# Optimization experiments

Measured on AMD Instinct MI355X. Metric: run time of the kernel, lower is better.

Reference implementation:

```python
import jax, jax.numpy as jnp
import numpy as np

T = 2048      # total tokens (single prefill sequence)
HID = 2048    # hidden_size
H = 16        # num k-heads == num v-heads
DK = 128      # key head dim
DV = 128      # value head dim
K = 4         # causal conv kernel width
EPS = 1e-6


def setup_inputs() -> dict:
    key = jax.random.key(0)
    ks = jax.random.split(key, 10)
    n = lambda k, shape, sc: (jax.random.normal(k, shape, jnp.float32) * sc)
    return {
        "hidden_states": n(ks[0], (T, HID), 1.0),
        "Wq": n(ks[1], (HID, H * DK), 0.02),
        "Wk": n(ks[2], (HID, H * DK), 0.02),
        "Wv": n(ks[3], (HID, H * DV), 0.02),
        "Wb": n(ks[4], (HID, H), 0.02),
        "conv_wq": n(ks[5], (H * DK, K), 0.5),
        "conv_wk": n(ks[6], (H * DK, K), 0.5),
        "conv_wv": n(ks[7], (H * DV, K), 0.5),
        "o_norm_w": jnp.ones((DV,), jnp.float32),
        "Wo": n(ks[8], (HID, HID), 0.02),
    }


def _causal_conv_silu(x, w):
    # x: [T, D], w: [D, K] depthwise causal conv, then SiLU (matches causal_conv1d_fn)
    xp = jnp.pad(x, ((K - 1, 0), (0, 0)))
    y = sum(xp[j:j + T] * w[:, j] for j in range(K))
    return jax.nn.silu(y)


def _l2norm(x):
    return x * jax.lax.rsqrt(jnp.sum(x * x, axis=-1, keepdims=True) + EPS)


def reference(hidden_states, Wq, Wk, Wv, Wb, conv_wq, conv_wk, conv_wv, o_norm_w, Wo):
    # projections [T, H*D]
    q = _causal_conv_silu(hidden_states @ Wq, conv_wq).reshape(T, H, DK)
    k = _causal_conv_silu(hidden_states @ Wk, conv_wk).reshape(T, H, DK)
    v = _causal_conv_silu(hidden_states @ Wv, conv_wv).reshape(T, H, DV)
    beta = jax.nn.sigmoid(hidden_states @ Wb)  # [T, H]

    # qk l2-norm + scale (FLA chunk_delta_rule defaults)
    q = _l2norm(q) * (DK ** -0.5)
    k = _l2norm(k)

    # delta-rule recurrence: S <- S + beta * k (v - k^T S)
    def step(S, inp):
        q_t, k_t, v_t, b_t = inp            # [H,DK],[H,DK],[H,DV],[H]
        kS = jnp.einsum('hk,hkv->hv', k_t, S)
        delta = b_t[:, None] * (v_t - kS)   # [H, DV]
        S = S + jnp.einsum('hk,hv->hkv', k_t, delta)
        o_t = jnp.einsum('hk,hkv->hv', q_t, S)
        return S, o_t

    S0 = jnp.zeros((H, DK, DV), jnp.float32)
    _, o = jax.lax.scan(step, S0, (q, k, v, beta))  # o: [T, H, DV]

    # per-head RMSNorm on value head dim
    o = o * jax.lax.rsqrt(jnp.mean(o * o, axis=-1, keepdims=True) + EPS) * o_norm_w
    out = o.reshape(T, H * DV) @ Wo
    return out
```

## Files before the change

kernel.cpp:

```cpp
#include <hip/hip_runtime.h>

typedef unsigned short u16;
typedef __attribute__((ext_vector_type(4))) unsigned short u16x4;
typedef __attribute__((ext_vector_type(8))) unsigned short u16x8;
typedef __attribute__((ext_vector_type(8))) short short8;
typedef __attribute__((ext_vector_type(4))) float f32x4;

#define DEVI __device__ __forceinline__

DEVI u16 f2b(float f) {
  union { float f; unsigned u; } x; x.f = f;
  unsigned r = (x.u + 0x7fffu + ((x.u >> 16) & 1u)) >> 16;
  return (u16)r;
}
DEVI float b2f(u16 h) {
  union { unsigned u; float f; } x; x.u = ((unsigned)h) << 16;
  return x.f;
}
DEVI f32x4 mfma_bf16(short8 a, short8 b, f32x4 c) {
  return __builtin_amdgcn_mfma_f32_16x16x32_bf16(a, b, c, 0, 0, 0);
}
DEVI void gl2lds16(const u16* g, u16* l) {
  __builtin_amdgcn_global_load_lds((__attribute__((address_space(1))) void*)g,
                                   (__attribute__((address_space(3))) void*)l,
                                   16, 0, 0);
}
DEVI void barrier_lds() {
  asm volatile("s_waitcnt lgkmcnt(0)\n\ts_barrier" ::: "memory");
}

__global__ void k_cvt(const float* __restrict__ src, u16* __restrict__ dst, int n4,
                      const float* __restrict__ Wb, u16* __restrict__ WbT) {
  int b = blockIdx.x;
  if (b < 4096) {
    int i = b * 256 + threadIdx.x;
    if (i < n4) {
      float4 v = ((const float4*)src)[i];
      u16x4 r; r.x = f2b(v.x); r.y = f2b(v.y); r.z = f2b(v.z); r.w = f2b(v.w);
      ((u16x4*)dst)[i] = r;
    }
  } else {
    int j = (b - 4096) * 256 + threadIdx.x;
    int n = j >> 11, k = j & 2047;
    WbT[j] = f2b(Wb[k * 16 + n]);
  }
}

__global__ __launch_bounds__(256)
void k_transpose4(const float* __restrict__ s0, const float* __restrict__ s1,
                  const float* __restrict__ s2, const float* __restrict__ s3,
                  u16* __restrict__ d0, u16* __restrict__ d1,
                  u16* __restrict__ d2, u16* __restrict__ d3) {
  const int RC = 2048;
  const float* src = (blockIdx.z == 0) ? s0 : (blockIdx.z == 1) ? s1 : (blockIdx.z == 2) ? s2 : s3;
  u16* dst = (blockIdx.z == 0) ? d0 : (blockIdx.z == 1) ? d1 : (blockIdx.z == 2) ? d2 : d3;
  __shared__ u16 tile[64 * 66];
  int bx = blockIdx.x << 6, by = blockIdx.y << 6;
  int x = threadIdx.x & 63, g = threadIdx.x >> 6;
#pragma unroll
  for (int i = 0; i < 16; ++i) {
    int r = (i << 2) + g;
    tile[x * 66 + r] = f2b(src[(size_t)(by + r) * RC + bx + x]);
  }
  __syncthreads();
#pragma unroll
  for (int i = 0; i < 16; ++i) {
    int r = (i << 2) + g;
    dst[(size_t)(bx + r) * RC + by + x] = tile[r * 66 + x];
  }
}


struct StageCtx { size_t go[2]; int lo[2]; };

DEVI void stage_half(const u16* g, const StageCtx& sc, u16* l) {
  gl2lds16(g + sc.go[0], l + sc.lo[0]);
  gl2lds16(g + sc.go[1], l + sc.lo[1]);
}

DEVI void rdA(const u16* h, const int (&aoff)[4][2], short8 (&a)[4][2]) {
#pragma unroll
  for (int m = 0; m < 4; ++m) {
    a[m][0] = *(const short8*)(h + aoff[m][0]);
    a[m][1] = *(const short8*)(h + aoff[m][1]);
  }
}
DEVI void rdB(const u16* h, const int (&boff)[2][2], short8 (&b)[2][2]) {
#pragma unroll
  for (int n = 0; n < 2; ++n) {
    b[n][0] = *(const short8*)(h + boff[n][0]);
    b[n][1] = *(const short8*)(h + boff[n][1]);
  }
}

template <int QA, int QB>
DEVI void mmquad(const short8 (&a)[4][2], const short8 (&b)[2][2], f32x4 (&acc)[8][4]) {
  __builtin_amdgcn_s_setprio(1);
#pragma unroll
  for (int m = 0; m < 4; ++m)
#pragma unroll
    for (int n = 0; n < 2; ++n) {
      acc[(QA << 2) + m][(QB << 1) + n] =
          mfma_bf16(a[m][0], b[n][0], acc[(QA << 2) + m][(QB << 1) + n]);
      acc[(QA << 2) + m][(QB << 1) + n] =
          mfma_bf16(a[m][1], b[n][1], acc[(QA << 2) + m][(QB << 1) + n]);
    }
  __builtin_amdgcn_s_setprio(0);
}

template <int MODE>
DEVI void ktile(u16* lds, int u,
                const u16* gA0, const u16* gA1, const u16* gB0, const u16* gB1,
                const StageCtx& sc,
                const int (&aoff)[4][2], const int (&boff)[2][2],
                f32x4 (&acc)[8][4]) {
  const int cs = (u & 1) << 13, ns = ((u + 1) & 1) << 13;
  const size_t uo1 = (size_t)(u + 1) << 6, uo2 = (size_t)(u + 2) << 6;
  short8 a0[4][2], a1[4][2], b0[2][2], b1[2][2];
  rdA(lds + cs, aoff, a0);
  rdB(lds + 32768 + cs, boff, b0);
  if constexpr (MODE <= 1) stage_half(gA1 + uo1, sc, lds + 16384 + ns);
  asm volatile("s_waitcnt lgkmcnt(8)" ::: "memory");
  __builtin_amdgcn_s_barrier();
  asm volatile("s_waitcnt lgkmcnt(0)" ::: "memory");
  __builtin_amdgcn_sched_barrier(0);
  mmquad<0, 0>(a0, b0, acc);
  __builtin_amdgcn_s_barrier();
  rdB(lds + 49152 + cs, boff, b1);
  if constexpr (MODE == 0) stage_half(gA0 + uo2, sc, lds + cs);
  __builtin_amdgcn_s_barrier();
  asm volatile("s_waitcnt lgkmcnt(0)" ::: "memory");
  __builtin_amdgcn_sched_barrier(0);
  mmquad<0, 1>(a0, b1, acc);
  __builtin_amdgcn_s_barrier();
  rdA(lds + 16384 + cs, aoff, a1);
  if constexpr (MODE == 0) stage_half(gB0 + uo2, sc, lds + 32768 + cs);
  __builtin_amdgcn_s_barrier();
  asm volatile("s_waitcnt lgkmcnt(0)" ::: "memory");
  __builtin_amdgcn_sched_barrier(0);
  mmquad<1, 0>(a1, b0, acc);
  __builtin_amdgcn_s_barrier();
  if constexpr (MODE == 0) {
    stage_half(gB1 + uo2, sc, lds + 49152 + cs);
    asm volatile("s_waitcnt vmcnt(6)" ::: "memory");
  }
  if constexpr (MODE == 1) asm volatile("s_waitcnt vmcnt(0)" ::: "memory");
  __builtin_amdgcn_s_barrier();
  mmquad<1, 1>(a1, b1, acc);
  __builtin_amdgcn_s_barrier();
}

template <int FOUT>
__global__ __launch_bounds__(512, 2)
void k_gemm8p(const u16* __restrict__ A, const u16* __restrict__ BT,
              u16* __restrict__ Cb, float* __restrict__ Cf,
              int N, int K, int NT, size_t czstride) {
  __shared__ __align__(16) u16 lds[65536];
  const int tid = threadIdx.x, wave = tid >> 6, lane = tid & 63;
  const int wm = wave >> 2, wn = wave & 3;
  const int fr = lane & 15, fq = (lane >> 4) << 4;
  const long bm = (long)blockIdx.y << 8, bn = (long)blockIdx.x << 8;
  const int kz = blockIdx.z;
  int aoff[4][2], boff[2][2];
#pragma unroll
  for (int m = 0; m < 4; ++m)
#pragma unroll
    for (int ks = 0; ks < 2; ++ks) {
      int row = (wm << 6) + (m << 4) + fr;
      int kb = (ks << 6) + fq;
      aoff[m][ks] = (row << 6) + ((kb ^ ((fr & 7) << 4)) >> 1);
    }
#pragma unroll
  for (int n = 0; n < 2; ++n)
#pragma unroll
    for (int ks = 0; ks < 2; ++ks) {
      int row = (wn << 5) + (n << 4) + fr;
      int kb = (ks << 6) + fq;
      boff[n][ks] = (row << 6) + ((kb ^ ((fr & 7) << 4)) >> 1);
    }
  StageCtx sc;
#pragma unroll
  for (int s = 0; s < 2; ++s) {
    int c = (s << 9) + tid, row = c >> 3;
    int kbs = (((c & 7) << 4) ^ ((row & 7) << 4));
    sc.go[s] = (size_t)row * K + (kbs >> 1);
    sc.lo[s] = ((s << 9) + (tid & ~63)) << 3;
  }
  const size_t kbase = (size_t)kz * ((size_t)NT << 6);
  const u16* gA0 = A + (size_t)bm * K + kbase;
  const u16* gA1 = gA0 + (size_t)128 * K;
  const u16* gB0 = BT + (size_t)bn * K + kbase;
  const u16* gB1 = gB0 + (size_t)128 * K;
  f32x4 acc[8][4];
#pragma unroll
  for (int i = 0; i < 8; ++i)
#pragma unroll
    for (int j = 0; j < 4; ++j) acc[i][j] = (f32x4){0.f, 0.f, 0.f, 0.f};
  stage_half(gA0, sc, lds + 0);
  stage_half(gA1, sc, lds + 16384);
  stage_half(gB0, sc, lds + 32768);
  stage_half(gB1, sc, lds + 49152);
  stage_half(gA0 + 64, sc, lds + 8192);
  stage_half(gB0 + 64, sc, lds + 32768 + 8192);
  stage_half(gB1 + 64, sc, lds + 49152 + 8192);
  asm volatile("s_waitcnt vmcnt(6)" ::: "memory");
  __builtin_amdgcn_s_barrier();
  for (int u = 0; u + 2 < NT; ++u)
    ktile<0>(lds, u, gA0, gA1, gB0, gB1, sc, aoff, boff, acc);
  ktile<1>(lds, NT - 2, gA0, gA1, gB0, gB1, sc, aoff, boff, acc);
  ktile<2>(lds, NT - 1, gA0, gA1, gB0, gB1, sc, aoff, boff, acc);
  const int er = (lane >> 4) << 2, ec = lane & 15;
  float* cf = Cf + (size_t)kz * czstride;
#pragma unroll
  for (int ai = 0; ai < 8; ++ai) {
    long row0 = bm + ((long)(ai >> 2) << 7) + (wm << 6) + ((ai & 3) << 4) + er;
#pragma unroll
    for (int bj = 0; bj < 4; ++bj) {
      long col = bn + ((long)(bj >> 1) << 7) + (wn << 5) + ((bj & 1) << 4) + ec;
#pragma unroll
      for (int r = 0; r < 4; ++r) {
        if (FOUT) cf[(size_t)(row0 + r) * N + col] = acc[ai][bj][r];
        else      Cb[(size_t)(row0 + r) * N + col] = f2b(acc[ai][bj][r]);
      }
    }
  }
}

__global__ __launch_bounds__(256)
void k_add4(const float* __restrict__ p, float* __restrict__ out, size_t stride4) {
  size_t i = (size_t)blockIdx.x * 256 + threadIdx.x;
  const float4* p4 = (const float4*)p;
  float4 a = p4[i], b = p4[i + stride4], c = p4[i + 2 * stride4], d = p4[i + 3 * stride4];
  float4 r;
  r.x = (a.x + b.x) + (c.x + d.x);
  r.y = (a.y + b.y) + (c.y + d.y);
  r.z = (a.z + b.z) + (c.z + d.z);
  r.w = (a.w + b.w) + (c.w + d.w);
  ((float4*)out)[i] = r;
}

__global__ __launch_bounds__(256, 4)
void k_beta(const u16* __restrict__ Xb, const u16* __restrict__ WbT,
            float* __restrict__ beta) {
  __shared__ float part[4][256];
  int tid = threadIdx.x, w = tid >> 6, lane = tid & 63;
  int t0 = blockIdx.x << 4;
  int fr = lane & 15, fq = (lane >> 4) << 3;
  const u16* ap = Xb + (size_t)(t0 + fr) * 2048 + (w << 9) + fq;
  const u16* bp = WbT + (size_t)fr * 2048 + (w << 9) + fq;
  f32x4 acc = {0.f, 0.f, 0.f, 0.f};
#pragma unroll
  for (int ks = 0; ks < 16; ++ks)
    acc = mfma_bf16(*(const short8*)(ap + (ks << 5)), *(const short8*)(bp + (ks << 5)), acc);
  int er = (lane >> 4) << 2;
#pragma unroll
  for (int r = 0; r < 4; ++r) part[w][(er + r) * 16 + fr] = acc[r];
  __syncthreads();
  float s = part[0][tid] + part[1][tid] + part[2][tid] + part[3][tid];
  beta[(t0 << 4) + tid] = 1.f / (1.f + __expf(-s));
}

__global__ __launch_bounds__(256, 4)
void k_conv(const u16* __restrict__ qkv,
            const float* __restrict__ cwq, const float* __restrict__ cwk,
            const float* __restrict__ cwv,
            u16* __restrict__ qn, u16* __restrict__ kn, u16* __restrict__ vn) {
  __shared__ __align__(16) u16 xs[67 * 136];
  __shared__ float wf[128 * 4];
  int tt = blockIdx.x, s = blockIdx.y;
  int kind = s >> 4, h = s & 15;
  int t0 = tt << 6;
  int col = (kind << 11) + (h << 7);
  int tid = threadIdx.x;
  const float* cw = (kind == 0) ? cwq : ((kind == 1) ? cwk : cwv);
  if (tid < 128) *(float4*)&wf[tid << 2] = *(const float4*)(cw + (size_t)((h << 7) + tid) * 4);
  for (int i = tid; i < 1072; i += 256) {
    int prow = i >> 4, c8 = (i & 15) << 3;
    int g = t0 - 3 + prow;
    u16x8 v = {0, 0, 0, 0, 0, 0, 0, 0};
    if (g >= 0) v = *(const u16x8*)(qkv + (size_t)g * 6144 + col + c8);
    *(u16x8*)&xs[prow * 136 + c8] = v;
  }
  __syncthreads();
  int t = tid >> 2, dg = tid & 3;
  float y[32];
  float ss = 0.f;
#pragma unroll
  for (int e8 = 0; e8 < 4; ++e8) {
    int d0 = (dg << 5) + (e8 << 3);
    u16x8 a0 = *(const u16x8*)&xs[(t + 0) * 136 + d0];
    u16x8 a1 = *(const u16x8*)&xs[(t + 1) * 136 + d0];
    u16x8 a2 = *(const u16x8*)&xs[(t + 2) * 136 + d0];
    u16x8 a3 = *(const u16x8*)&xs[(t + 3) * 136 + d0];
#pragma unroll
    for (int e = 0; e < 8; ++e) {
      float4 w = *(const float4*)&wf[(d0 + e) << 2];
      float v = b2f(a0[e]) * w.x + b2f(a1[e]) * w.y + b2f(a2[e]) * w.z + b2f(a3[e]) * w.w;
      v = v / (1.f + __expf(-v));
      y[(e8 << 3) + e] = v;
      ss += v * v;
    }
  }
  float sc = 1.f;
  if (kind < 2) {
    ss += __shfl_xor(ss, 1);
    ss += __shfl_xor(ss, 2);
    sc = rsqrtf(ss + 1e-6f);
    if (kind == 0) sc *= 0.08838834764831843f;
  }
  u16* dst = (kind == 0) ? qn : ((kind == 1) ? kn : vn);
  u16* dp = dst + ((size_t)h << 18) + ((size_t)(t0 + t) << 7) + (dg << 5);
#pragma unroll
  for (int e8 = 0; e8 < 4; ++e8) {
    u16x8 p;
#pragma unroll
    for (int e = 0; e < 8; ++e) p[e] = f2b(y[(e8 << 3) + e] * sc);
    *(u16x8*)(dp + (e8 << 3)) = p;
  }
}

__global__ __launch_bounds__(256, 2)
void k_prep(const u16* __restrict__ qn, const u16* __restrict__ kn, const u16* __restrict__ vn,
            const float* __restrict__ beta,
            u16* __restrict__ Gg, u16* __restrict__ Wg,
            u16* __restrict__ KTg, u16* __restrict__ UTg) {
  __shared__ __align__(16) char sm[70912];
  u16*  Kc  = (u16*)sm;
  u16*  Qc  = (u16*)(sm + 17408);
  u16*  Vc  = (u16*)(sm + 34816);
  u16*  KTl = (u16*)(sm + 52224);
  float* AL = (float*)(sm + 52224);
  float* Bl = (float*)(sm + 70656);
  u16*  WR  = Qc;
  int h = blockIdx.x, c = blockIdx.y;
  int tid = threadIdx.x, wave = tid >> 6, lane = tid & 63;
  size_t ch = (size_t)(c * 16 + h);
  const u16* kb = kn + ((size_t)h << 18) + ((size_t)c << 13);
  const u16* qb = qn + ((size_t)h << 18) + ((size_t)c << 13);
  const u16* vb = vn + ((size_t)h << 18) + ((size_t)c << 13);
#pragma unroll
  for (int s = 0; s < 4; ++s) {
    int e = (tid + (s << 8)) << 3;
    int t = e >> 7, d = e & 127;
    *(u16x8*)&Kc[t * 136 + d] = *(const u16x8*)(kb + e);
    *(u16x8*)&Qc[t * 136 + d] = *(const u16x8*)(qb + e);
    *(u16x8*)&Vc[t * 136 + d] = *(const u16x8*)(vb + e);
  }
  if (tid < 64) Bl[tid] = beta[((c << 6) + tid) * 16 + h];
  __syncthreads();
  int fr = lane & 15, fq = (lane >> 4) << 3, q4 = (lane >> 4) << 2;
  int arow = (wave << 4) + fr;
  f32x4 kk[4], qk[4];
#pragma unroll
  for (int ct = 0; ct < 4; ++ct) { kk[ct] = (f32x4){0.f,0.f,0.f,0.f}; qk[ct] = (f32x4){0.f,0.f,0.f,0.f}; }
#pragma unroll
  for (int ks = 0; ks < 4; ++ks) {
    short8 aK = *(const short8*)&Kc[arow * 136 + (ks << 5) + fq];
    short8 aQ = *(const short8*)&Qc[arow * 136 + (ks << 5) + fq];
#pragma unroll
    for (int ct = 0; ct < 4; ++ct) {
      short8 bK = *(const short8*)&Kc[((ct << 4) + fr) * 136 + (ks << 5) + fq];
      kk[ct] = mfma_bf16(aK, bK, kk[ct]);
      qk[ct] = mfma_bf16(aQ, bK, qk[ct]);
    }
  }
#pragma unroll
  for (int ct = 0; ct < 4; ++ct)
#pragma unroll
    for (int r = 0; r < 4; ++r) {
      int i = (wave << 4) + q4 + r, j = (ct << 4) + fr;
      Gg[(ch << 12) + i * 64 + j] = f2b((j <= i) ? qk[ct][r] : 0.f);
    }
  {
    int d = tid & 127, tg = tid >> 7;
#pragma unroll
    for (int it = 0; it < 4; ++it) {
      int t0 = (tg + (it << 1)) << 3;
      u16x8 pk;
#pragma unroll
      for (int j = 0; j < 8; ++j) pk[j] = Kc[(t0 + j) * 136 + d];
      *(u16x8*)&KTl[d * 72 + t0] = pk;
    }
  }
  __syncthreads();
#pragma unroll
  for (int it = 0; it < 4; ++it) {
    int idx = tid + (it << 8);
    int row = idx >> 3, j8 = (idx & 7) << 3;
    *(u16x8*)(KTg + (ch << 13) + (row << 6) + j8) = *(const u16x8*)&KTl[row * 72 + j8];
  }
  __syncthreads();
  {
    float bi[4];
#pragma unroll
    for (int r = 0; r < 4; ++r) bi[r] = Bl[(wave << 4) + q4 + r];
#pragma unroll
    for (int ct = 0; ct < 4; ++ct)
#pragma unroll
      for (int r = 0; r < 4; ++r) {
        int i = (wave << 4) + q4 + r, j = (ct << 4) + fr;
        AL[i * 64 + j] = (j < i) ? bi[r] * kk[ct][r] : 0.f;
      }
  }
  __syncthreads();
  float X[64];
  {
    const u16* colp = (tid < 128) ? (Kc + tid) : (Vc + (tid - 128));
#pragma unroll
    for (int t = 0; t < 64; ++t) X[t] = Bl[t] * b2f(colp[t * 136]);
#pragma unroll
    for (int r = 1; r < 64; ++r) {
      float s = 0.f;
      const float* Ar = &AL[r * 64];
      int r4 = r & ~3;
#pragma unroll
      for (int l = 0; l < 64; l += 4)
        if (l + 4 <= r) {
          float4 a = *(const float4*)(Ar + l);
          s += a.x * X[l] + a.y * X[l + 1] + a.z * X[l + 2] + a.w * X[l + 3];
        }
#pragma unroll
      for (int l = 0; l < 4; ++l)
        if (r4 + l < r) s += Ar[r4 + l] * X[r4 + l];
      X[r] -= s;
    }
  }
  __syncthreads();
  if (tid < 128) {
#pragma unroll
    for (int t = 0; t < 64; ++t) WR[t * 136 + tid] = f2b(X[t]);
  } else {
    int v = tid - 128;
    u16* dstr = UTg + (ch << 13) + (v << 6);
#pragma unroll
    for (int j = 0; j < 8; ++j) {
      u16x8 p;
#pragma unroll
      for (int e = 0; e < 8; ++e) p[e] = f2b(X[(j << 3) + e]);
      *(u16x8*)(dstr + (j << 3)) = p;
    }
  }
  __syncthreads();
#pragma unroll
  for (int it = 0; it < 4; ++it) {
    int idx = tid + (it << 8);
    int row = idx >> 4, j8 = (idx & 15) << 3;
    *(u16x8*)(Wg + (ch << 13) + (row << 7) + j8) = *(const u16x8*)&WR[row * 136 + j8];
  }
}

struct Frags { short8 q[4], w[4], g[2], k[4]; u16x4 u; };

DEVI void load_frags(Frags& f, const u16* qh, const u16* Wg, const u16* Gg,
                     const u16* KTg, const u16* UTg, int c, int h,
                     int trow, int fr, int fq, int q4, int w, int vbase) {
  const u16* qb = qh + ((size_t)((c << 6) + trow + fr) << 7) + fq;
#pragma unroll
  for (int ks = 0; ks < 4; ++ks) f.q[ks] = *(const short8*)(qb + (ks << 5));
  size_t ch = (size_t)(c * 16 + h);
  const u16* wb = Wg + (ch << 13) + ((size_t)(trow + fr) << 7) + fq;
#pragma unroll
  for (int ks = 0; ks < 4; ++ks) f.w[ks] = *(const short8*)(wb + (ks << 5));
  const u16* gb = Gg + (ch << 12) + ((size_t)(trow + fr) << 6) + fq;
#pragma unroll
  for (int ks = 0; ks < 2; ++ks) f.g[ks] = *(const short8*)(gb + (ks << 5));
  const u16* kbp = KTg + (ch << 13) + ((size_t)(w << 5) << 6) + fq;
#pragma unroll
  for (int dt = 0; dt < 2; ++dt)
#pragma unroll
    for (int ks = 0; ks < 2; ++ks)
      f.k[(dt << 1) | ks] = *(const short8*)(kbp + ((size_t)((dt << 4) + fr) << 6) + (ks << 5));
  f.u = *(const u16x4*)(UTg + (ch << 13) + ((size_t)(vbase + fr) << 6) + trow + q4);
}

DEVI void chunk_body(int c, Frags& f, u16* ST, u16* DT, u16* oh,
                     int trow, int fr, int fq, int q4, int w, int vbase,
                     f32x4& S0, f32x4& S1) {
#pragma unroll
  for (int r = 0; r < 4; ++r) {
    ST[(q4 + r) * 136 + (w << 5) + fr] = f2b(S0[r]);
    ST[(q4 + r) * 136 + (w << 5) + 16 + fr] = f2b(S1[r]);
  }
  barrier_lds();
  short8 sf[4];
#pragma unroll
  for (int ks = 0; ks < 4; ++ks) sf[ks] = *(const short8*)&ST[fr * 136 + (ks << 5) + fq];
  f32x4 racc = {0.f,0.f,0.f,0.f}, oacc = {0.f,0.f,0.f,0.f};
#pragma unroll
  for (int ks = 0; ks < 4; ++ks) {
    racc = mfma_bf16(f.w[ks], sf[ks], racc);
    oacc = mfma_bf16(f.q[ks], sf[ks], oacc);
  }
#pragma unroll
  for (int r = 0; r < 4; ++r)
    DT[fr * 72 + trow + q4 + r] = f2b(b2f(f.u[r]) - racc[r]);
  barrier_lds();
  short8 df[2];
#pragma unroll
  for (int ks = 0; ks < 2; ++ks) df[ks] = *(const short8*)&DT[fr * 72 + (ks << 5) + fq];
#pragma unroll
  for (int ks = 0; ks < 2; ++ks) {
    oacc = mfma_bf16(f.g[ks], df[ks], oacc);
    S0 = mfma_bf16(df[ks], f.k[ks], S0);
    S1 = mfma_bf16(df[ks], f.k[2 | ks], S1);
  }
#pragma unroll
  for (int r = 0; r < 4; ++r)
    oh[(size_t)((c << 6) + trow + q4 + r) * 128 + vbase + fr] = f2b(oacc[r]);
}

__global__ __launch_bounds__(256, 1)
void k_delta(const u16* __restrict__ qn, const u16* __restrict__ Wg,
             const u16* __restrict__ Gg, const u16* __restrict__ KTg,
             const u16* __restrict__ UTg, u16* __restrict__ o) {
  __shared__ __align__(16) u16 ST[16 * 136];
  __shared__ __align__(16) u16 DT[16 * 72];
  int bx = blockIdx.x;
  int h = bx & 15, vbase = (bx >> 4) << 4;
  int tid = threadIdx.x, w = tid >> 6, lane = tid & 63;
  int fr = lane & 15, fq = (lane >> 4) << 3, q4 = (lane >> 4) << 2;
  int trow = w << 4;
  const u16* qh = qn + ((size_t)h << 18);
  u16* oh = o + ((size_t)h << 18);
  f32x4 S0 = {0.f,0.f,0.f,0.f}, S1 = {0.f,0.f,0.f,0.f};
  Frags fa, fb;
  load_frags(fa, qh, Wg, Gg, KTg, UTg, 0, h, trow, fr, fq, q4, w, vbase);
  for (int c = 0; c < 32; c += 2) {
    int c1 = c + 1, c2 = (c + 2 < 32) ? c + 2 : 31;
    load_frags(fb, qh, Wg, Gg, KTg, UTg, c1, h, trow, fr, fq, q4, w, vbase);
    chunk_body(c, fa, ST, DT, oh, trow, fr, fq, q4, w, vbase, S0, S1);
    load_frags(fa, qh, Wg, Gg, KTg, UTg, c2, h, trow, fr, fq, q4, w, vbase);
    chunk_body(c1, fb, ST, DT, oh, trow, fr, fq, q4, w, vbase, S0, S1);
  }
}

__global__ __launch_bounds__(256, 4)
void k_onorm(const u16* __restrict__ o, const float* __restrict__ onw,
             u16* __restrict__ onb) {
  __shared__ float wl[128];
  int tt = blockIdx.x, h = blockIdx.y, tid = threadIdx.x;
  if (tid < 128) wl[tid] = onw[tid];
  __syncthreads();
  int t = tid >> 2, dg = tid & 3;
  const u16* src = o + ((size_t)h << 18) + ((size_t)((tt << 6) + t) << 7) + (dg << 5);
  u16x8 a[4];
  float ss = 0.f;
#pragma unroll
  for (int e8 = 0; e8 < 4; ++e8) {
    a[e8] = *(const u16x8*)(src + (e8 << 3));
#pragma unroll
    for (int e = 0; e < 8; ++e) { float x = b2f(a[e8][e]); ss += x * x; }
  }
  ss += __shfl_xor(ss, 1);
  ss += __shfl_xor(ss, 2);
  float inv = rsqrtf(ss * (1.f / 128.f) + 1e-6f);
  u16* dp = onb + ((size_t)((tt << 6) + t) << 11) + (h << 7) + (dg << 5);
#pragma unroll
  for (int e8 = 0; e8 < 4; ++e8) {
    u16x8 p;
#pragma unroll
    for (int e = 0; e < 8; ++e)
      p[e] = f2b(b2f(a[e8][e]) * inv * wl[(dg << 5) + (e8 << 3) + e]);
    *(u16x8*)(dp + (e8 << 3)) = p;
  }
}

extern "C" void kernel_launch(void* const* d_in, const int* in_sizes, int n_in,
                              void* d_out, int out_size, void* d_ws, size_t ws_size,
                              hipStream_t stream) {
  (void)in_sizes; (void)n_in; (void)out_size; (void)ws_size;
  const float* hs  = (const float*)d_in[0];
  const float* Wq  = (const float*)d_in[1];
  const float* Wk  = (const float*)d_in[2];
  const float* Wv  = (const float*)d_in[3];
  const float* Wb  = (const float*)d_in[4];
  const float* cwq = (const float*)d_in[5];
  const float* cwk = (const float*)d_in[6];
  const float* cwv = (const float*)d_in[7];
  const float* onw = (const float*)d_in[8];
  const float* Wo  = (const float*)d_in[9];
  float* out = (float*)d_out;
  char* ws = (char*)d_ws;
  const size_t MB = 1ull << 20;
  u16*  Xb   = (u16*)(ws);
  u16*  WT   = (u16*)(ws + 8  * MB);
  u16*  WoT  = (u16*)(ws + 32 * MB);
  u16*  QKV  = (u16*)(ws + 40 * MB);
  u16*  Wg   = (u16*)(ws + 40 * MB);
  u16*  KTg  = (u16*)(ws + 48 * MB);
  u16*  UTg  = (u16*)(ws + 56 * MB);
  u16*  qn_  = (u16*)(ws + 64 * MB);
  u16*  kn_  = (u16*)(ws + 72 * MB);
  u16*  vn_  = (u16*)(ws + 80 * MB);
  float* beta= (float*)(ws + 88 * MB);
  u16*  WbT  = (u16*)(ws + 88 * MB + 512 * 1024);
  u16*  Gm   = (u16*)(ws + 89 * MB);
  u16*  o_   = (u16*)(ws + 93 * MB);
  u16*  onb  = (u16*)(ws + 109 * MB);
  float* Pk  = (float*)(ws + 40 * MB);

  k_cvt<<<4224, 256, 0, stream>>>(hs, Xb, 2048 * 2048 / 4, Wb, WbT);
  k_transpose4<<<dim3(32, 32, 4), 256, 0, stream>>>(
      Wq, Wk, Wv, Wo, WT, WT + 2048 * 2048, WT + 2 * 2048 * 2048, WoT);
  k_gemm8p<0><<<dim3(24, 8, 1), 512, 0, stream>>>(Xb, WT, QKV, nullptr, 6144, 2048, 32, 0);
  k_beta<<<128, 256, 0, stream>>>(Xb, WbT, beta);
  k_conv<<<dim3(32, 48), 256, 0, stream>>>(QKV, cwq, cwk, cwv, qn_, kn_, vn_);
  k_prep<<<dim3(16, 32), 256, 0, stream>>>(qn_, kn_, vn_, beta, Gm, Wg, KTg, UTg);
  k_delta<<<128, 256, 0, stream>>>(qn_, Wg, Gm, KTg, UTg, o_);
  k_onorm<<<dim3(32, 16), 256, 0, stream>>>(o_, onw, onb);
  k_gemm8p<1><<<dim3(8, 8, 4), 512, 0, stream>>>(onb, WoT, nullptr, Pk, 2048, 2048, 8,
                                                 (size_t)2048 * 2048);
  k_add4<<<4096, 256, 0, stream>>>(Pk, out, (size_t)2048 * 2048 / 4);
}
```

Measured before the change: 346.8 us.

## Software-pipeline LDS fragment reads in GEMM and fuse beta into QKV launch

The GEMM k-tile loop now keeps A/B register fragments across iterations. It prefetches the next tile's fragments from LDS during the last MFMA quad and drops several barriers and lgkmcnt waits, so LDS reads overlap matrix math. Separately, the beta projection is folded into the QKV GEMM launch as 64 extra blocks of 512 threads, removing one kernel launch and filling idle CUs. The reordering of stage_half and the waits adds risk of LDS races if the vmcnt counts are wrong, and it raises register pressure.

```diff
diff --git a/kernel.cpp b/kernel.cpp
--- a/kernel.cpp
+++ b/kernel.cpp
@@ -113,54 +113,45 @@
                 const u16* gA0, const u16* gA1, const u16* gB0, const u16* gB1,
                 const StageCtx& sc,
                 const int (&aoff)[4][2], const int (&boff)[2][2],
+                short8 (&a0)[4][2], short8 (&a1)[4][2],
+                short8 (&b0)[2][2], short8 (&b1)[2][2],
                 f32x4 (&acc)[8][4]) {
   const int cs = (u & 1) << 13, ns = ((u + 1) & 1) << 13;
+  const u16* A1c = lds + 16384 + cs;
+  const u16* B1c = lds + 49152 + cs;
   const size_t uo1 = (size_t)(u + 1) << 6, uo2 = (size_t)(u + 2) << 6;
-  short8 a0[4][2], a1[4][2], b0[2][2], b1[2][2];
-  rdA(lds + cs, aoff, a0);
-  rdB(lds + 32768 + cs, boff, b0);
+  __builtin_amdgcn_s_barrier();
+  rdB(B1c, boff, b1);
   if constexpr (MODE <= 1) stage_half(gA1 + uo1, sc, lds + 16384 + ns);
-  asm volatile("s_waitcnt lgkmcnt(8)" ::: "memory");
-  __builtin_amdgcn_s_barrier();
-  asm volatile("s_waitcnt lgkmcnt(0)" ::: "memory");
-  __builtin_amdgcn_sched_barrier(0);
   mmquad<0, 0>(a0, b0, acc);
   __builtin_amdgcn_s_barrier();
-  rdB(lds + 49152 + cs, boff, b1);
+  rdA(A1c, aoff, a1);
   if constexpr (MODE == 0) stage_half(gA0 + uo2, sc, lds + cs);
-  __builtin_amdgcn_s_barrier();
-  asm volatile("s_waitcnt lgkmcnt(0)" ::: "memory");
-  __builtin_amdgcn_sched_barrier(0);
   mmquad<0, 1>(a0, b1, acc);
   __builtin_amdgcn_s_barrier();
-  rdA(lds + 16384 + cs, aoff, a1);
   if constexpr (MODE == 0) stage_half(gB0 + uo2, sc, lds + 32768 + cs);
-  __builtin_amdgcn_s_barrier();
-  asm volatile("s_waitcnt lgkmcnt(0)" ::: "memory");
-  __builtin_amdgcn_sched_barrier(0);
   mmquad<1, 0>(a1, b0, acc);
-  __builtin_amdgcn_s_barrier();
-  if constexpr (MODE == 0) {
-    stage_half(gB1 + uo2, sc, lds + 49152 + cs);
-    asm volatile("s_waitcnt vmcnt(6)" ::: "memory");
-  }
+  if constexpr (MODE == 0) asm volatile("s_waitcnt vmcnt(4)" ::: "memory");
   if constexpr (MODE == 1) asm volatile("s_waitcnt vmcnt(0)" ::: "memory");
   __builtin_amdgcn_s_barrier();
+  if constexpr (MODE <= 1) {
+    rdA(lds + ns, aoff, a0);
+    rdB(lds + 32768 + ns, boff, b0);
+  }
+  if constexpr (MODE == 0) stage_half(gB1 + uo2, sc, lds + 49152 + cs);
   mmquad<1, 1>(a1, b1, acc);
-  __builtin_amdgcn_s_barrier();
 }
 
 template <int FOUT>
-__global__ __launch_bounds__(512, 2)
-void k_gemm8p(const u16* __restrict__ A, const u16* __restrict__ BT,
-              u16* __restrict__ Cb, float* __restrict__ Cf,
-              int N, int K, int NT, size_t czstride) {
+DEVI void gemm8p_body(const u16* __restrict__ A, const u16* __restrict__ BT,
+                      u16* __restrict__ Cb, float* __restrict__ Cf,
+                      int N, int K, int NT, size_t czstride,
+                      int ibx, int iby, int ikz) {
   __shared__ __align__(16) u16 lds[65536];
   const int tid = threadIdx.x, wave = tid >> 6, lane = tid & 63;
   const int wm = wave >> 2, wn = wave & 3;
   const int fr = lane & 15, fq = (lane >> 4) << 4;
-  const long bm = (long)blockIdx.y << 8, bn = (long)blockIdx.x << 8;
-  const int kz = blockIdx.z;
+  const long bm = (long)iby << 8, bn = (long)ibx << 8;
   int aoff[4][2], boff[2][2];
 #pragma unroll
   for (int m = 0; m < 4; ++m)
@@ -186,7 +177,7 @@
     sc.go[s] = (size_t)row * K + (kbs >> 1);
     sc.lo[s] = ((s << 9) + (tid & ~63)) << 3;
   }
-  const size_t kbase = (size_t)kz * ((size_t)NT << 6);
+  const size_t kbase = (size_t)ikz * ((size_t)NT << 6);
   const u16* gA0 = A + (size_t)bm * K + kbase;
   const u16* gA1 = gA0 + (size_t)128 * K;
   const u16* gB0 = BT + (size_t)bn * K + kbase;
@@ -196,6 +187,7 @@
   for (int i = 0; i < 8; ++i)
 #pragma unroll
     for (int j = 0; j < 4; ++j) acc[i][j] = (f32x4){0.f, 0.f, 0.f, 0.f};
+  short8 a0[4][2], a1[4][2], b0[2][2], b1[2][2];
   stage_half(gA0, sc, lds + 0);
   stage_half(gA1, sc, lds + 16384);
   stage_half(gB0, sc, lds + 32768);
@@ -205,12 +197,14 @@
   stage_half(gB1 + 64, sc, lds + 49152 + 8192);
   asm volatile("s_waitcnt vmcnt(6)" ::: "memory");
   __builtin_amdgcn_s_barrier();
+  rdA(lds + 0, aoff, a0);
+  rdB(lds + 32768, boff, b0);
   for (int u = 0; u + 2 < NT; ++u)
-    ktile<0>(lds, u, gA0, gA1, gB0, gB1, sc, aoff, boff, acc);
-  ktile<1>(lds, NT - 2, gA0, gA1, gB0, gB1, sc, aoff, boff, acc);
-  ktile<2>(lds, NT - 1, gA0, gA1, gB0, gB1, sc, aoff, boff, acc);
+    ktile<0>(lds, u, gA0, gA1, gB0, gB1, sc, aoff, boff, a0, a1, b0, b1, acc);
+  ktile<1>(lds, NT - 2, gA0, gA1, gB0, gB1, sc, aoff, boff, a0, a1, b0, b1, acc);
+  ktile<2>(lds, NT - 1, gA0, gA1, gB0, gB1, sc, aoff, boff, a0, a1, b0, b1, acc);
   const int er = (lane >> 4) << 2, ec = lane & 15;
-  float* cf = Cf + (size_t)kz * czstride;
+  float* cf = Cf + (size_t)ikz * czstride;
 #pragma unroll
   for (int ai = 0; ai < 8; ++ai) {
     long row0 = bm + ((long)(ai >> 2) << 7) + (wm << 6) + ((ai & 3) << 4) + er;
@@ -224,6 +218,52 @@
       }
     }
   }
+}
+
+DEVI void beta_body(const u16* __restrict__ Xb, const u16* __restrict__ WbT,
+                    float* __restrict__ beta, int bb) {
+  __shared__ float part[8][256];
+  int tid = threadIdx.x, w = tid >> 6, lane = tid & 63;
+  int fr = lane & 15, fq = (lane >> 4) << 3;
+#pragma unroll
+  for (int it = 0; it < 2; ++it) {
+    int t0 = (bb << 5) + (it << 4);
+    const u16* ap = Xb + (size_t)(t0 + fr) * 2048 + (w << 8) + fq;
+    const u16* bp = WbT + (size_t)fr * 2048 + (w << 8) + fq;
+    f32x4 acc = {0.f, 0.f, 0.f, 0.f};
+#pragma unroll
+    for (int ks = 0; ks < 8; ++ks)
+      acc = mfma_bf16(*(const short8*)(ap + (ks << 5)), *(const short8*)(bp + (ks << 5)), acc);
+    int er = (lane >> 4) << 2;
+#pragma unroll
+    for (int r = 0; r < 4; ++r) part[w][(er + r) * 16 + fr] = acc[r];
+    __syncthreads();
+    if (tid < 256) {
+      float s = 0.f;
+#pragma unroll
+      for (int j = 0; j < 8; ++j) s += part[j][tid];
+      beta[(t0 << 4) + tid] = 1.f / (1.f + __expf(-s));
+    }
+    __syncthreads();
+  }
+}
+
+__global__ __launch_bounds__(512, 2)
+void k_qkv_beta(const u16* __restrict__ Xb, const u16* __restrict__ WT,
+                u16* __restrict__ QKV, const u16* __restrict__ WbT,
+                float* __restrict__ beta) {
+  int bid = blockIdx.x;
+  if (bid < 192)
+    gemm8p_body<0>(Xb, WT, QKV, nullptr, 6144, 2048, 32, 0, bid % 24, bid / 24, 0);
+  else
+    beta_body(Xb, WbT, beta, bid - 192);
+}
+
+__global__ __launch_bounds__(512, 2)
+void k_gemm_wo8p(const u16* __restrict__ A, const u16* __restrict__ BT,
+                 float* __restrict__ Cf, int N, int K, int NT, size_t czstride) {
+  gemm8p_body<1>(A, BT, nullptr, Cf, N, K, NT, czstride,
+                 blockIdx.x, blockIdx.y, blockIdx.z);
 }
 
 __global__ __launch_bounds__(256)
@@ -237,27 +277,6 @@
   r.z = (a.z + b.z) + (c.z + d.z);
   r.w = (a.w + b.w) + (c.w + d.w);
   ((float4*)out)[i] = r;
-}
-
-__global__ __launch_bounds__(256, 4)
-void k_beta(const u16* __restrict__ Xb, const u16* __restrict__ WbT,
-            float* __restrict__ beta) {
-  __shared__ float part[4][256];
-  int tid = threadIdx.x, w = tid >> 6, lane = tid & 63;
-  int t0 = blockIdx.x << 4;
-  int fr = lane & 15, fq = (lane >> 4) << 3;
-  const u16* ap = Xb + (size_t)(t0 + fr) * 2048 + (w << 9) + fq;
-  const u16* bp = WbT + (size_t)fr * 2048 + (w << 9) + fq;
-  f32x4 acc = {0.f, 0.f, 0.f, 0.f};
-#pragma unroll
-  for (int ks = 0; ks < 16; ++ks)
-    acc = mfma_bf16(*(const short8*)(ap + (ks << 5)), *(const short8*)(bp + (ks << 5)), acc);
-  int er = (lane >> 4) << 2;
-#pragma unroll
-  for (int r = 0; r < 4; ++r) part[w][(er + r) * 16 + fr] = acc[r];
-  __syncthreads();
-  float s = part[0][tid] + part[1][tid] + part[2][tid] + part[3][tid];
-  beta[(t0 << 4) + tid] = 1.f / (1.f + __expf(-s));
 }
 
 __global__ __launch_bounds__(256, 4)
@@ -602,13 +621,12 @@
   k_cvt<<<4224, 256, 0, stream>>>(hs, Xb, 2048 * 2048 / 4, Wb, WbT);
   k_transpose4<<<dim3(32, 32, 4), 256, 0, stream>>>(
       Wq, Wk, Wv, Wo, WT, WT + 2048 * 2048, WT + 2 * 2048 * 2048, WoT);
-  k_gemm8p<0><<<dim3(24, 8, 1), 512, 0, stream>>>(Xb, WT, QKV, nullptr, 6144, 2048, 32, 0);
-  k_beta<<<128, 256, 0, stream>>>(Xb, WbT, beta);
+  k_qkv_beta<<<256, 512, 0, stream>>>(Xb, WT, QKV, WbT, beta);
   k_conv<<<dim3(32, 48), 256, 0, stream>>>(QKV, cwq, cwk, cwv, qn_, kn_, vn_);
   k_prep<<<dim3(16, 32), 256, 0, stream>>>(qn_, kn_, vn_, beta, Gm, Wg, KTg, UTg);
   k_delta<<<128, 256, 0, stream>>>(qn_, Wg, Gm, KTg, UTg, o_);
   k_onorm<<<dim3(32, 16), 256, 0, stream>>>(o_, onw, onb);
-  k_gemm8p<1><<<dim3(8, 8, 4), 512, 0, stream>>>(onb, WoT, nullptr, Pk, 2048, 2048, 8,
+  k_gemm_wo8p<<<dim3(8, 8, 4), 512, 0, stream>>>(onb, WoT, Pk, 2048, 2048, 8,
                                                  (size_t)2048 * 2048);
   k_add4<<<4096, 256, 0, stream>>>(Pk, out, (size_t)2048 * 2048 / 4);
 }
```

After: 348.3 us. About the same (+0.4%).
